# Performance work log

Hardware: AMD Instinct MI355X
Metric: run time of the kernel (lower is better)

The kernel has to match this reference:

```python
import jax, jax.numpy as jnp
import numpy as np

L, B, E = 8192, 2, 1024
H, WS = 16, 256
D = E // H


def setup_inputs() -> dict:
    key = jax.random.key(0)
    ks = jax.random.split(key, 8)
    mk = lambda k: jax.random.normal(k, (E, E), dtype=jnp.float32) * 0.02
    return {
        'query': jax.random.normal(ks[0], (L, B, E), dtype=jnp.float32),
        'key':   jax.random.normal(ks[1], (L, B, E), dtype=jnp.float32),
        'value': jax.random.normal(ks[2], (L, B, E), dtype=jnp.float32),
        'Wq': mk(ks[3]), 'bq': jnp.zeros((E,), jnp.float32),
        'Wk': mk(ks[4]), 'bk': jnp.zeros((E,), jnp.float32),
        'Wv': mk(ks[5]), 'bv': jnp.zeros((E,), jnp.float32),
        'Wo': mk(ks[6]), 'bo': jnp.zeros((E,), jnp.float32),
    }


def reference(query, key, value, Wq, bq, Wk, bk, Wv, bv, Wo, bo):
    # Faithful translation, including the original's (B,L,H,D) layout and the
    # raw-memory view(B,H,L//ws,ws,D) reinterpretation of that layout.
    proj = lambda x, W, b: x @ W.T + b
    # (L,B,E) -> (L,B,H,D) -> transpose(0,1) -> (B,L,H,D)
    q = jnp.swapaxes(proj(query, Wq, bq).reshape(L, B, H, D), 0, 1)
    k = jnp.swapaxes(proj(key,   Wk, bk).reshape(L, B, H, D), 0, 1)
    v = jnp.swapaxes(proj(value, Wv, bv).reshape(L, B, H, D), 0, 1)
    # L > ws, L % ws == 0 -> pad_len = 0; contiguous().view == reshape
    nW = L // WS
    q = q.reshape(B, H, nW, WS, D)
    k = k.reshape(B, H, nW, WS, D)
    v = v.reshape(B, H, nW, WS, D)
    attn = jnp.einsum('bhnqd,bhnkd->bhnqk', q, k) / (D ** 0.5)
    attn = jax.nn.softmax(attn, axis=-1)
    out = jnp.einsum('bhnqk,bhnkd->bhnqd', attn, v)  # (B,H,nW,ws,D)
    out = out.reshape(B, H, L, D)
    # transpose(0,1).contiguous().view(L,B,E): reinterpret (H,B,L,D) memory
    out = jnp.swapaxes(out, 0, 1).reshape(L, B, E)
    return out @ Wo.T + bo
```

## Files before the change

kernel.cpp:

```cpp
#include <hip/hip_runtime.h>


typedef _Float16 half8 __attribute__((ext_vector_type(8)));
typedef _Float16 half4 __attribute__((ext_vector_type(4)));
typedef float    f32x4 __attribute__((ext_vector_type(4)));

#define MFMA16(a, b, c) __builtin_amdgcn_mfma_f32_16x16x32_f16((a), (b), (c), 0, 0, 0)
#define VM(n) asm volatile("s_waitcnt vmcnt(" #n ")" ::: "memory")
#define SCHED0 __builtin_amdgcn_sched_barrier(0)
#define LGKM0 do { asm volatile("s_waitcnt lgkmcnt(0)" ::: "memory"); SCHED0; } while (0)
#define BARW do { __builtin_amdgcn_s_barrier(); SCHED0; } while (0)

__device__ inline void gload16(const _Float16* g, _Float16* l) {
  __builtin_amdgcn_global_load_lds(
      (const __attribute__((address_space(1))) void*)g,
      (__attribute__((address_space(3))) void*)l, 16, 0, 0);
}

__device__ inline half8 cvt8(float4 a, float4 b) {
  half8 h = {(_Float16)a.x, (_Float16)a.y, (_Float16)a.z, (_Float16)a.w,
             (_Float16)b.x, (_Float16)b.y, (_Float16)b.z, (_Float16)b.w};
  return h;
}

__global__ __launch_bounds__(256) void cvtw_k(const float* __restrict__ s0,
                                              const float* __restrict__ s1,
                                              const float* __restrict__ s2,
                                              const float* __restrict__ s3,
                                              _Float16* __restrict__ d) {
  const float* s = blockIdx.y == 0 ? s0 : blockIdx.y == 1 ? s1 : blockIdx.y == 2 ? s2 : s3;
  _Float16* dst = d + (size_t)blockIdx.y * (1 << 20);
  int i = (blockIdx.x * 256 + threadIdx.x) * 8;
  float4 a = *(const float4*)(s + i);
  float4 b = *(const float4*)(s + i + 4);
  *(half8*)(dst + i) = cvt8(a, b);
}

template <int A_F32, int OUT_F32>
__device__ __attribute__((always_inline)) void gemm8p_body(
    const void* __restrict__ A, const _Float16* __restrict__ Bw,
    const float* __restrict__ bias, void* __restrict__ Cout) {
  constexpr int K = 1024, NN = 1024, NT = 16;
  __shared__ alignas(16) _Float16 SH[65536];
  const int tid = threadIdx.x, lane = tid & 63, wave = tid >> 6;
  const int r15 = lane & 15, g = lane >> 4;
  const int wr = wave >> 2, wc = wave & 3;
  const int m0 = blockIdx.x * 256, n0 = blockIdx.y * 256;

  const int sp = tid >> 3;
  const int sv = (tid & 7) ^ (sp & 7);
  const int srow = 2 * sp + (sv >> 2);
  const int scol = (sv & 3) * 8;
  const int sdst = tid * 8;

  const int rp = r15 >> 1, rsub = r15 & 1;
  const int rslot = ((rsub * 4 + g) ^ rp) * 8;

  const float* Af = (const float*)A;
  const _Float16* Ah = (const _Float16*)A;

  f32x4 acc[8][4] = {};
  float4 fr0[4], fr1[4];
  half8 af[4], bf[4];

#define A_REGION(buf, kh) (&SH[(buf)*16384 + (kh)*8192])
#define B_REGION(buf, kh) (&SH[32768 + (buf)*16384 + (kh)*8192])

#define STAGE_B(t, buf, kh)                                                    \
  do {                                                                         \
    const _Float16* _s = Bw + (size_t)(n0 + srow) * K + (t)*64 + (kh)*32 + scol; \
    gload16(_s, B_REGION(buf, kh) + sdst);                                     \
    gload16(_s + (size_t)128 * K, B_REGION(buf, kh) + sdst + 4096);            \
  } while (0)

#define STAGE_A16(t, buf, kh)                                                  \
  do {                                                                         \
    const _Float16* _s = Ah + (size_t)(m0 + srow) * K + (t)*64 + (kh)*32 + scol; \
    gload16(_s, A_REGION(buf, kh) + sdst);                                     \
    gload16(_s + (size_t)128 * K, A_REGION(buf, kh) + sdst + 4096);            \
  } while (0)

#define A_ISSUE(fr, t, kh)                                                     \
  do {                                                                         \
    const float* _s = Af + (size_t)(m0 + srow) * K + (t)*64 + (kh)*32 + scol;  \
    fr[0] = ((const float4*)_s)[0];                                            \
    fr[1] = ((const float4*)_s)[1];                                            \
    const float* _s2 = _s + (size_t)128 * K;                                   \
    fr[2] = ((const float4*)_s2)[0];                                           \
    fr[3] = ((const float4*)_s2)[1];                                           \
  } while (0)

#define A_WRITE(fr, buf, kh)                                                   \
  do {                                                                         \
    *(half8*)&A_REGION(buf, kh)[sdst] = cvt8(fr[0], fr[1]);                    \
    *(half8*)&A_REGION(buf, kh)[sdst + 4096] = cvt8(fr[2], fr[3]);             \
  } while (0)

#define READ_AF(buf, kk, MH)                                                   \
  do {                                                                         \
    _Float16* _b = A_REGION(buf, kk);                                          \
    int _pb = (wr * 64 + (MH)*32 + rp) * 64 + rslot;                           \
    af[0] = *(half8*)&_b[_pb];                                                 \
    af[1] = *(half8*)&_b[_pb + 512];                                           \
    af[2] = *(half8*)&_b[_pb + 1024];                                          \
    af[3] = *(half8*)&_b[_pb + 1536];                                          \
  } while (0)

#define READ_BF(buf, kk)                                                       \
  do {                                                                         \
    _Float16* _b = B_REGION(buf, kk);                                          \
    int _pb = (wc * 32 + rp) * 64 + rslot;                                     \
    bf[0] = *(half8*)&_b[_pb];                                                 \
    bf[1] = *(half8*)&_b[_pb + 512];                                           \
    bf[2] = *(half8*)&_b[_pb + 1024];                                          \
    bf[3] = *(half8*)&_b[_pb + 1536];                                          \
  } while (0)

#define MFMA_Q(MH)                                                             \
  do {                                                                         \
    __builtin_amdgcn_s_setprio(1);                                             \
    _Pragma("unroll") for (int mi = 0; mi < 4; mi++)                           \
        _Pragma("unroll") for (int ni = 0; ni < 4; ni++) acc[(MH)*4 + mi][ni] = \
        MFMA16(af[mi], bf[ni], acc[(MH)*4 + mi][ni]);                          \
    __builtin_amdgcn_s_setprio(0);                                             \
  } while (0)

  if (A_F32) {
    A_ISSUE(fr0, 0, 0);
    A_ISSUE(fr1, 0, 1);
    STAGE_B(0, 0, 0);
    STAGE_B(0, 0, 1);
    VM(8); SCHED0;
    A_WRITE(fr0, 0, 0);
    VM(4); SCHED0;
    A_WRITE(fr1, 0, 1);
    asm volatile("s_waitcnt lgkmcnt(0)" ::: "memory");
  } else {
    STAGE_A16(0, 0, 0);
    STAGE_A16(0, 0, 1);
    STAGE_B(0, 0, 0);
    STAGE_B(0, 0, 1);
  }

  for (int t = 0; t < NT - 1; t++) {
    const int buf = t & 1, nb = buf ^ 1;
    if (A_F32) {
      A_ISSUE(fr0, t + 1, 0);
      VM(6);
    } else {
      STAGE_A16(t + 1, nb, 0);
      VM(4);
    }
    BARW;
    READ_AF(buf, 0, 0);
    READ_BF(buf, 0);
    LGKM0;
    MFMA_Q(0);
    if (A_F32) A_ISSUE(fr1, t + 1, 1);
    else STAGE_A16(t + 1, nb, 1);
    READ_AF(buf, 0, 1);
    LGKM0;
    MFMA_Q(1);
    STAGE_B(t + 1, nb, 0);
    VM(6); SCHED0;
    if (A_F32) A_WRITE(fr0, nb, 0);
    BARW;
    READ_AF(buf, 1, 0);
    READ_BF(buf, 1);
    LGKM0;
    MFMA_Q(0);
    STAGE_B(t + 1, nb, 1);
    if (A_F32) {
      VM(4); SCHED0;
      A_WRITE(fr1, nb, 1);
    }
    READ_AF(buf, 1, 1);
    LGKM0;
    MFMA_Q(1);
  }

  {
    VM(2);
    BARW;
    READ_AF(1, 0, 0);
    READ_BF(1, 0);
    LGKM0;
    MFMA_Q(0);
    READ_AF(1, 0, 1);
    LGKM0;
    MFMA_Q(1);
    VM(0);
    BARW;
    READ_AF(1, 1, 0);
    READ_BF(1, 1);
    LGKM0;
    MFMA_Q(0);
    READ_AF(1, 1, 1);
    LGKM0;
    MFMA_Q(1);
  }

#pragma unroll
  for (int ni = 0; ni < 4; ni++) {
    const int col = n0 + wc * 64 + ni * 16 + r15;
    const float bv = bias[col];
#pragma unroll
    for (int mi8 = 0; mi8 < 8; mi8++) {
      const int rowb = m0 + wr * 128 + mi8 * 16 + g * 4;
#pragma unroll
      for (int r = 0; r < 4; r++) {
        float x = acc[mi8][ni][r] + bv;
        if (OUT_F32)
          ((float*)Cout)[(size_t)(rowb + r) * NN + col] = x;
        else
          ((_Float16*)Cout)[(size_t)(rowb + r) * NN + col] = (_Float16)x;
      }
    }
  }
#undef A_REGION
#undef B_REGION
#undef STAGE_B
#undef STAGE_A16
#undef A_ISSUE
#undef A_WRITE
#undef READ_AF
#undef READ_BF
#undef MFMA_Q
}

__global__ __launch_bounds__(512) void gemm_proj_k(
    const float* __restrict__ Aq, const float* __restrict__ Ak,
    const float* __restrict__ Av, const _Float16* __restrict__ W16,
    const float* __restrict__ bq, const float* __restrict__ bk,
    const float* __restrict__ bv, _Float16* __restrict__ Oq,
    _Float16* __restrict__ Ok, _Float16* __restrict__ Ov) {
  const int z = blockIdx.z;
  const float* A = z == 0 ? Aq : z == 1 ? Ak : Av;
  const float* bias = z == 0 ? bq : z == 1 ? bk : bv;
  _Float16* out = z == 0 ? Oq : z == 1 ? Ok : Ov;
  gemm8p_body<1, 0>((const void*)A, W16 + ((size_t)z << 20), bias, (void*)out);
}

__global__ __launch_bounds__(512) void gemm_out_k(const _Float16* __restrict__ A,
                                                  const _Float16* __restrict__ Bw,
                                                  const float* __restrict__ bias,
                                                  float* __restrict__ Cout) {
  gemm8p_body<0, 1>((const void*)A, Bw, bias, (void*)Cout);
}

__global__ __launch_bounds__(256) void vtrans_k(const _Float16* __restrict__ Vp,
                                                _Float16* __restrict__ Vt) {
  const int c = blockIdx.x, b = blockIdx.y;
  __shared__ alignas(16) _Float16 Vl[256 * 64];
  const int tid = threadIdx.x;
  const int l0 = c * 16;
#pragma unroll
  for (int i = 0; i < 8; i++) {
    int q = tid + i * 256;
    int w = q >> 3, ck = q & 7;
    int ls = l0 + (w >> 4), h = w & 15;
    half8 v = *(const half8*)(Vp + (size_t)(ls * 2 + b) * 1024 + h * 64 + ck * 8);
    *(half8*)&Vl[w * 64 + (ck ^ (w & 7)) * 8] = v;
  }
  __syncthreads();
  const int d = tid >> 2, kcq = tid & 3;
  const size_t obase = ((size_t)(b * 512 + c) * 64 + d) * 256 + kcq * 64;
#pragma unroll
  for (int i8 = 0; i8 < 8; i8++) {
    half8 v;
#pragma unroll
    for (int j = 0; j < 8; j++) {
      int k = kcq * 64 + i8 * 8 + j;
      v[j] = Vl[k * 64 + (((d >> 3) ^ (k & 7)) * 8) + (d & 7)];
    }
    *(half8*)(Vt + obase + i8 * 8) = v;
  }
}

__global__ __launch_bounds__(512) void attn_win_k(const _Float16* __restrict__ Qp,
                                                  const _Float16* __restrict__ Kp,
                                                  const _Float16* __restrict__ Vt,
                                                  _Float16* __restrict__ Y) {
  const int c = blockIdx.x, b = blockIdx.y;
  __shared__ alignas(16) _Float16 Kl[256 * 64];
  __shared__ alignas(16) _Float16 Vl[64 * 256];
  const int tid = threadIdx.x, lane = tid & 63, wave = tid >> 6;
  const int i15 = lane & 15, g = lane >> 4;
  const int l0 = c * 16;

#pragma unroll
  for (int i = 0; i < 4; i++) {
    int q = tid + i * 512;
    int w = q >> 3, ck = q & 7;
    int ls = l0 + (w >> 4), h = w & 15;
    half8 v = *(const half8*)(Kp + (size_t)(ls * 2 + b) * 1024 + h * 64 + ck * 8);
    *(half8*)&Kl[w * 64 + (ck ^ (w & 7)) * 8] = v;
  }
  const size_t vb0 = (size_t)(b * 512 + c) * 64 * 256;
#pragma unroll
  for (int i = 0; i < 4; i++) {
    int q = tid + i * 512;
    int d = q >> 5, ck = q & 31;
    half8 v = *(const half8*)(Vt + vb0 + (size_t)d * 256 + ck * 8);
    *(half8*)&Vl[d * 256 + (ck ^ ((d & 7) << 2)) * 8] = v;
  }
  half8 qf[2][2];
#pragma unroll
  for (int wf = 0; wf < 2; wf++)
#pragma unroll
    for (int dh = 0; dh < 2; dh++) {
      int ls = l0 + wave * 2 + wf;
      qf[wf][dh] =
          *(const half8*)(Qp + (size_t)(ls * 2 + b) * 1024 + i15 * 64 + dh * 32 + g * 8);
    }
  __syncthreads();

  f32x4 acc[16][2] = {};
#pragma unroll
  for (int m = 0; m < 16; m++) {
    int row = m * 16 + i15;
    half8 a0 = *(half8*)&Kl[row * 64 + ((g) ^ (i15 & 7)) * 8];
    half8 a1 = *(half8*)&Kl[row * 64 + ((4 + g) ^ (i15 & 7)) * 8];
    acc[m][0] = MFMA16(a0, qf[0][0], acc[m][0]);
    acc[m][0] = MFMA16(a1, qf[0][1], acc[m][0]);
    acc[m][1] = MFMA16(a0, qf[1][0], acc[m][1]);
    acc[m][1] = MFMA16(a1, qf[1][1], acc[m][1]);
  }

#pragma unroll
  for (int wf = 0; wf < 2; wf++) {
    float mx = -3.0e38f;
#pragma unroll
    for (int m = 0; m < 16; m++)
#pragma unroll
      for (int r = 0; r < 4; r++) mx = fmaxf(mx, acc[m][wf][r]);
    mx = fmaxf(mx, __shfl_xor(mx, 16, 64));
    mx = fmaxf(mx, __shfl_xor(mx, 32, 64));
    float sum = 0.f;
#pragma unroll
    for (int m = 0; m < 16; m++)
#pragma unroll
      for (int r = 0; r < 4; r++) {
        float e = __expf((acc[m][wf][r] - mx) * 0.125f);
        acc[m][wf][r] = e;
        sum += e;
      }
    sum += __shfl_xor(sum, 16, 64);
    sum += __shfl_xor(sum, 32, 64);
    float inv = 1.f / sum;
#pragma unroll
    for (int m = 0; m < 16; m++)
#pragma unroll
      for (int r = 0; r < 4; r++) acc[m][wf][r] *= inv;
  }
  __syncthreads();

  _Float16* Pw = &Kl[wave * 2048];
  f32x4 oacc[2][4] = {};
#pragma unroll
  for (int kq = 0; kq < 4; kq++) {
#pragma unroll
    for (int wf = 0; wf < 2; wf++) {
      int rrow = wf * 16 + i15;
#pragma unroll
      for (int ml = 0; ml < 4; ml++) {
        f32x4 pv = acc[kq * 4 + ml][wf];
        half4 h = {(_Float16)pv[0], (_Float16)pv[1], (_Float16)pv[2], (_Float16)pv[3]};
        int ck = ml * 2 + (g >> 1);
        *(half4*)&Pw[rrow * 64 + ((ck ^ (i15 & 7)) * 8) + (g & 1) * 4] = h;
      }
    }
    asm volatile("s_waitcnt lgkmcnt(0)" ::: "memory");
    __builtin_amdgcn_sched_barrier(0);
#pragma unroll
    for (int kfl = 0; kfl < 2; kfl++) {
      half8 pa0 = *(half8*)&Pw[(i15)*64 + (((kfl * 4 + g) ^ (i15 & 7)) * 8)];
      half8 pa1 = *(half8*)&Pw[(16 + i15) * 64 + (((kfl * 4 + g) ^ (i15 & 7)) * 8)];
#pragma unroll
      for (int df = 0; df < 4; df++) {
        int drow = df * 16 + i15;
        half8 vbf =
            *(half8*)&Vl[drow * 256 + (((kq * 8 + kfl * 4 + g) ^ ((i15 & 7) << 2)) * 8)];
        oacc[0][df] = MFMA16(pa0, vbf, oacc[0][df]);
        oacc[1][df] = MFMA16(pa1, vbf, oacc[1][df]);
      }
    }
  }

  const int h2 = c >> 5, n = c & 31;
  const size_t yb = ((size_t)(h2 * 2 + b) * 8192 + (size_t)n * 256) * 64;
#pragma unroll
  for (int wf = 0; wf < 2; wf++)
#pragma unroll
    for (int df = 0; df < 4; df++)
#pragma unroll
      for (int r = 0; r < 4; r++) {
        int w = wave * 32 + wf * 16 + g * 4 + r;
        Y[yb + (size_t)w * 64 + df * 16 + i15] = (_Float16)oacc[wf][df][r];
      }
}

extern "C" void kernel_launch(void* const* d_in, const int* in_sizes, int n_in,
                              void* d_out, int out_size, void* d_ws, size_t ws_size,
                              hipStream_t stream) {
  const float* query = (const float*)d_in[0];
  const float* key_ = (const float*)d_in[1];
  const float* value = (const float*)d_in[2];
  const float* Wq = (const float*)d_in[3];
  const float* bq = (const float*)d_in[4];
  const float* Wk = (const float*)d_in[5];
  const float* bk = (const float*)d_in[6];
  const float* Wv = (const float*)d_in[7];
  const float* bv = (const float*)d_in[8];
  const float* Wo = (const float*)d_in[9];
  const float* bo = (const float*)d_in[10];

  _Float16* ws = (_Float16*)d_ws;
  _Float16* W16 = ws;
  _Float16* W16o = W16 + 3 * (1 << 20);
  _Float16* Vp = ws + 4 * (1 << 20);
  _Float16* Vt = Vp + (1 << 24);
  _Float16* Ybuf = Vp;

  _Float16* Qp = (_Float16*)d_out;
  _Float16* Kp = Qp + (1 << 24);

  cvtw_k<<<dim3(512, 4), 256, 0, stream>>>(Wq, Wk, Wv, Wo, W16);

  gemm_proj_k<<<dim3(64, 4, 3), 512, 0, stream>>>(query, key_, value, W16, bq, bk, bv,
                                                  Qp, Kp, Vp);

  vtrans_k<<<dim3(512, 2), 256, 0, stream>>>(Vp, Vt);
  attn_win_k<<<dim3(512, 2), 512, 0, stream>>>(Qp, Kp, Vt, Ybuf);

  gemm_out_k<<<dim3(64, 4), 512, 0, stream>>>(Ybuf, W16o, bo, (float*)d_out);

  (void)in_sizes; (void)n_in; (void)out_size; (void)ws_size;
}
```

Baseline: 255.0 us.

## Deepen fp32-A register prefetch to two tiles ahead in projection GEMM

The fp32-input path of the projection GEMM now keeps two sets of register staging buffers (even/odd) and issues global loads for tile t+2 while tile t+1's data is converted and written to LDS. The K loop is fully unrolled into 16 tile steps with specialized tail modes and adjusted vmcnt waits. The aim is to hide global-load latency of the fp32 activations behind more MFMA work. It doubles the staging registers, which could raise register pressure and lower occupancy, and it hardcodes 16 K-tiles.

```diff
diff --git a/kernel.cpp b/kernel.cpp
--- a/kernel.cpp
+++ b/kernel.cpp
@@ -60,7 +60,6 @@
   const _Float16* Ah = (const _Float16*)A;
 
   f32x4 acc[8][4] = {};
-  float4 fr0[4], fr1[4];
   half8 af[4], bf[4];
 
 #define A_REGION(buf, kh) (&SH[(buf)*16384 + (kh)*8192])
@@ -125,79 +124,97 @@
     __builtin_amdgcn_s_setprio(0);                                             \
   } while (0)
 
+#define TILE_F32(T, BUF, FRX0, FRX1, FRY0, FRY1, MODE)                         \
+  {                                                                            \
+    const int _t = (T), _nb = (BUF) ^ 1;                                       \
+                                                                      \
+    if (MODE < 2) STAGE_B(_t + 1, _nb, 0);                                     \
+    if (MODE < 2) { VM(12); } else { VM(2); }                                  \
+    SCHED0; BARW;                                                              \
+    READ_AF(BUF, 0, 0); READ_BF(BUF, 0); LGKM0; MFMA_Q(0);                     \
+                                                                      \
+    if (MODE == 0) A_ISSUE(FRX0, _t + 2, 0);                                   \
+    READ_AF(BUF, 0, 1); LGKM0; MFMA_Q(1);                                      \
+                                                                      \
+    if (MODE < 2) STAGE_B(_t + 1, _nb, 1);                                     \
+    if (MODE < 2) A_WRITE(FRY0, _nb, 0);                                       \
+    if (MODE == 0) { VM(12); } else if (MODE == 1) { VM(8); } else { VM(0); }  \
+    SCHED0; BARW;                                                              \
+    READ_AF(BUF, 1, 0); READ_BF(BUF, 1); LGKM0; MFMA_Q(0);                     \
+                                                                      \
+    if (MODE == 0) A_ISSUE(FRX1, _t + 2, 1);                                   \
+    if (MODE < 2) A_WRITE(FRY1, _nb, 1);                                       \
+    READ_AF(BUF, 1, 1); LGKM0; MFMA_Q(1);                                      \
+  }
+
   if (A_F32) {
-    A_ISSUE(fr0, 0, 0);
-    A_ISSUE(fr1, 0, 1);
+    float4 frE0[4], frE1[4], frO0[4], frO1[4];
+    A_ISSUE(frE0, 0, 0);
+    A_ISSUE(frE1, 0, 1);
     STAGE_B(0, 0, 0);
     STAGE_B(0, 0, 1);
-    VM(8); SCHED0;
-    A_WRITE(fr0, 0, 0);
-    VM(4); SCHED0;
-    A_WRITE(fr1, 0, 1);
-    asm volatile("s_waitcnt lgkmcnt(0)" ::: "memory");
+    A_WRITE(frE0, 0, 0);
+    A_WRITE(frE1, 0, 1);
+    A_ISSUE(frO0, 1, 0);
+    A_ISSUE(frO1, 1, 1);
+    LGKM0;
+    for (int tt = 0; tt < 7; tt++) {
+      const int te = tt * 2;
+      TILE_F32(te, 0, frE0, frE1, frO0, frO1, 0);
+      TILE_F32(te + 1, 1, frO0, frO1, frE0, frE1, 0);
+    }
+    TILE_F32(14, 0, frE0, frE1, frO0, frO1, 1);
+    TILE_F32(15, 1, frO0, frO1, frE0, frE1, 2);
   } else {
     STAGE_A16(0, 0, 0);
     STAGE_A16(0, 0, 1);
     STAGE_B(0, 0, 0);
     STAGE_B(0, 0, 1);
-  }
-
-  for (int t = 0; t < NT - 1; t++) {
-    const int buf = t & 1, nb = buf ^ 1;
-    if (A_F32) {
-      A_ISSUE(fr0, t + 1, 0);
-      VM(6);
-    } else {
+    for (int t = 0; t < NT - 1; t++) {
+      const int buf = t & 1, nb = buf ^ 1;
       STAGE_A16(t + 1, nb, 0);
       VM(4);
-    }
-    BARW;
-    READ_AF(buf, 0, 0);
-    READ_BF(buf, 0);
-    LGKM0;
-    MFMA_Q(0);
-    if (A_F32) A_ISSUE(fr1, t + 1, 1);
-    else STAGE_A16(t + 1, nb, 1);
-    READ_AF(buf, 0, 1);
-    LGKM0;
-    MFMA_Q(1);
-    STAGE_B(t + 1, nb, 0);
-    VM(6); SCHED0;
-    if (A_F32) A_WRITE(fr0, nb, 0);
-    BARW;
-    READ_AF(buf, 1, 0);
-    READ_BF(buf, 1);
-    LGKM0;
-    MFMA_Q(0);
-    STAGE_B(t + 1, nb, 1);
-    if (A_F32) {
-      VM(4); SCHED0;
-      A_WRITE(fr1, nb, 1);
-    }
-    READ_AF(buf, 1, 1);
-    LGKM0;
-    MFMA_Q(1);
-  }
-
-  {
-    VM(2);
-    BARW;
-    READ_AF(1, 0, 0);
-    READ_BF(1, 0);
-    LGKM0;
-    MFMA_Q(0);
-    READ_AF(1, 0, 1);
-    LGKM0;
-    MFMA_Q(1);
-    VM(0);
-    BARW;
-    READ_AF(1, 1, 0);
-    READ_BF(1, 1);
-    LGKM0;
-    MFMA_Q(0);
-    READ_AF(1, 1, 1);
-    LGKM0;
-    MFMA_Q(1);
+      SCHED0; BARW;
+      READ_AF(buf, 0, 0);
+      READ_BF(buf, 0);
+      LGKM0;
+      MFMA_Q(0);
+      STAGE_A16(t + 1, nb, 1);
+      READ_AF(buf, 0, 1);
+      LGKM0;
+      MFMA_Q(1);
+      STAGE_B(t + 1, nb, 0);
+      VM(6);
+      SCHED0; BARW;
+      READ_AF(buf, 1, 0);
+      READ_BF(buf, 1);
+      LGKM0;
+      MFMA_Q(0);
+      STAGE_B(t + 1, nb, 1);
+      READ_AF(buf, 1, 1);
+      LGKM0;
+      MFMA_Q(1);
+    }
+    {
+      VM(2);
+      SCHED0; BARW;
+      READ_AF(1, 0, 0);
+      READ_BF(1, 0);
+      LGKM0;
+      MFMA_Q(0);
+      READ_AF(1, 0, 1);
+      LGKM0;
+      MFMA_Q(1);
+      VM(0);
+      SCHED0; BARW;
+      READ_AF(1, 1, 0);
+      READ_BF(1, 1);
+      LGKM0;
+      MFMA_Q(0);
+      READ_AF(1, 1, 1);
+      LGKM0;
+      MFMA_Q(1);
+    }
   }
 
 #pragma unroll
@@ -226,6 +243,7 @@
 #undef READ_AF
 #undef READ_BF
 #undef MFMA_Q
+#undef TILE_F32
 }
 
 __global__ __launch_bounds__(512) void gemm_proj_k(
```

New measurement: 306.4 us. +20.1%, slower.

## Pre-convert activations to fp16 and run projections as separate fp16 GEMMs

Applied to the files above, without the earlier changes.

The projection GEMM no longer loads fp32 activations and converts them to fp16 inside its main loop. Each of query, key and value is now converted to fp16 by a separate kernel into a shared workspace, and that fp16 buffer is fed to the same async-LDS GEMM path already used for the output projection. This removes the register staging and in-loop conversion from the GEMM pipeline. In exchange it adds an extra full read and write pass over every activation. It also replaces the single fused 3-way launch with six launches that run one after another, so each projection GEMM grid is only 256 blocks.

```diff
diff --git a/kernel.cpp b/kernel.cpp
--- a/kernel.cpp
+++ b/kernel.cpp
@@ -21,6 +21,15 @@
   half8 h = {(_Float16)a.x, (_Float16)a.y, (_Float16)a.z, (_Float16)a.w,
              (_Float16)b.x, (_Float16)b.y, (_Float16)b.z, (_Float16)b.w};
   return h;
+}
+
+__global__ __launch_bounds__(256) void cvt_fp16_k(const float* __restrict__ src,
+                                                  _Float16* __restrict__ dst, int n) {
+  int i = (blockIdx.x * 256 + threadIdx.x) * 8;
+  if (i >= n) return;
+  float4 a = *(const float4*)(src + i);
+  float4 b = *(const float4*)(src + i + 4);
+  *(half8*)(dst + i) = cvt8(a, b);
 }
 
 __global__ __launch_bounds__(256) void cvtw_k(const float* __restrict__ s0,
@@ -36,10 +45,11 @@
   *(half8*)(dst + i) = cvt8(a, b);
 }
 
-template <int A_F32, int OUT_F32>
-__device__ __attribute__((always_inline)) void gemm8p_body(
-    const void* __restrict__ A, const _Float16* __restrict__ Bw,
-    const float* __restrict__ bias, void* __restrict__ Cout) {
+template <int OUT_F32>
+__global__ __launch_bounds__(512) void gemm8p_k(const _Float16* __restrict__ Ah,
+                                                const _Float16* __restrict__ Bw,
+                                                const float* __restrict__ bias,
+                                                void* __restrict__ Cout) {
   constexpr int K = 1024, NN = 1024, NT = 16;
   __shared__ alignas(16) _Float16 SH[65536];
   const int tid = threadIdx.x, lane = tid & 63, wave = tid >> 6;
@@ -56,11 +66,7 @@
   const int rp = r15 >> 1, rsub = r15 & 1;
   const int rslot = ((rsub * 4 + g) ^ rp) * 8;
 
-  const float* Af = (const float*)A;
-  const _Float16* Ah = (const _Float16*)A;
-
   f32x4 acc[8][4] = {};
-  float4 fr0[4], fr1[4];
   half8 af[4], bf[4];
 
 #define A_REGION(buf, kh) (&SH[(buf)*16384 + (kh)*8192])
@@ -78,22 +84,6 @@
     const _Float16* _s = Ah + (size_t)(m0 + srow) * K + (t)*64 + (kh)*32 + scol; \
     gload16(_s, A_REGION(buf, kh) + sdst);                                     \
     gload16(_s + (size_t)128 * K, A_REGION(buf, kh) + sdst + 4096);            \
-  } while (0)
-
-#define A_ISSUE(fr, t, kh)                                                     \
-  do {                                                                         \
-    const float* _s = Af + (size_t)(m0 + srow) * K + (t)*64 + (kh)*32 + scol;  \
-    fr[0] = ((const float4*)_s)[0];                                            \
-    fr[1] = ((const float4*)_s)[1];                                            \
-    const float* _s2 = _s + (size_t)128 * K;                                   \
-    fr[2] = ((const float4*)_s2)[0];                                           \
-    fr[3] = ((const float4*)_s2)[1];                                           \
-  } while (0)
-
-#define A_WRITE(fr, buf, kh)                                                   \
-  do {                                                                         \
-    *(half8*)&A_REGION(buf, kh)[sdst] = cvt8(fr[0], fr[1]);                    \
-    *(half8*)&A_REGION(buf, kh)[sdst + 4096] = cvt8(fr[2], fr[3]);             \
   } while (0)
 
 #define READ_AF(buf, kk, MH)                                                   \
@@ -125,63 +115,39 @@
     __builtin_amdgcn_s_setprio(0);                                             \
   } while (0)
 
-  if (A_F32) {
-    A_ISSUE(fr0, 0, 0);
-    A_ISSUE(fr1, 0, 1);
-    STAGE_B(0, 0, 0);
-    STAGE_B(0, 0, 1);
-    VM(8); SCHED0;
-    A_WRITE(fr0, 0, 0);
-    VM(4); SCHED0;
-    A_WRITE(fr1, 0, 1);
-    asm volatile("s_waitcnt lgkmcnt(0)" ::: "memory");
-  } else {
-    STAGE_A16(0, 0, 0);
-    STAGE_A16(0, 0, 1);
-    STAGE_B(0, 0, 0);
-    STAGE_B(0, 0, 1);
-  }
+  STAGE_A16(0, 0, 0);
+  STAGE_A16(0, 0, 1);
+  STAGE_B(0, 0, 0);
+  STAGE_B(0, 0, 1);
 
   for (int t = 0; t < NT - 1; t++) {
     const int buf = t & 1, nb = buf ^ 1;
-    if (A_F32) {
-      A_ISSUE(fr0, t + 1, 0);
-      VM(6);
-    } else {
-      STAGE_A16(t + 1, nb, 0);
-      VM(4);
-    }
-    BARW;
+    STAGE_A16(t + 1, nb, 0);
+    VM(4);
+    SCHED0; BARW;
     READ_AF(buf, 0, 0);
     READ_BF(buf, 0);
     LGKM0;
     MFMA_Q(0);
-    if (A_F32) A_ISSUE(fr1, t + 1, 1);
-    else STAGE_A16(t + 1, nb, 1);
+    STAGE_A16(t + 1, nb, 1);
     READ_AF(buf, 0, 1);
     LGKM0;
     MFMA_Q(1);
     STAGE_B(t + 1, nb, 0);
-    VM(6); SCHED0;
-    if (A_F32) A_WRITE(fr0, nb, 0);
-    BARW;
+    VM(6);
+    SCHED0; BARW;
     READ_AF(buf, 1, 0);
     READ_BF(buf, 1);
     LGKM0;
     MFMA_Q(0);
     STAGE_B(t + 1, nb, 1);
-    if (A_F32) {
-      VM(4); SCHED0;
-      A_WRITE(fr1, nb, 1);
-    }
     READ_AF(buf, 1, 1);
     LGKM0;
     MFMA_Q(1);
   }
-
   {
     VM(2);
-    BARW;
+    SCHED0; BARW;
     READ_AF(1, 0, 0);
     READ_BF(1, 0);
     LGKM0;
@@ -190,7 +156,7 @@
     LGKM0;
     MFMA_Q(1);
     VM(0);
-    BARW;
+    SCHED0; BARW;
     READ_AF(1, 1, 0);
     READ_BF(1, 1);
     LGKM0;
@@ -221,31 +187,9 @@
 #undef B_REGION
 #undef STAGE_B
 #undef STAGE_A16
-#undef A_ISSUE
-#undef A_WRITE
 #undef READ_AF
 #undef READ_BF
 #undef MFMA_Q
-}
-
-__global__ __launch_bounds__(512) void gemm_proj_k(
-    const float* __restrict__ Aq, const float* __restrict__ Ak,
-    const float* __restrict__ Av, const _Float16* __restrict__ W16,
-    const float* __restrict__ bq, const float* __restrict__ bk,
-    const float* __restrict__ bv, _Float16* __restrict__ Oq,
-    _Float16* __restrict__ Ok, _Float16* __restrict__ Ov) {
-  const int z = blockIdx.z;
-  const float* A = z == 0 ? Aq : z == 1 ? Ak : Av;
-  const float* bias = z == 0 ? bq : z == 1 ? bk : bv;
-  _Float16* out = z == 0 ? Oq : z == 1 ? Ok : Ov;
-  gemm8p_body<1, 0>((const void*)A, W16 + ((size_t)z << 20), bias, (void*)out);
-}
-
-__global__ __launch_bounds__(512) void gemm_out_k(const _Float16* __restrict__ A,
-                                                  const _Float16* __restrict__ Bw,
-                                                  const float* __restrict__ bias,
-                                                  float* __restrict__ Cout) {
-  gemm8p_body<0, 1>((const void*)A, Bw, bias, (void*)Cout);
 }
 
 __global__ __launch_bounds__(256) void vtrans_k(const _Float16* __restrict__ Vp,
@@ -417,9 +361,13 @@
 
   _Float16* ws = (_Float16*)d_ws;
   _Float16* W16 = ws;
+  _Float16* W16q = W16;
+  _Float16* W16k = W16 + (1 << 20);
+  _Float16* W16v = W16 + 2 * (1 << 20);
   _Float16* W16o = W16 + 3 * (1 << 20);
-  _Float16* Vp = ws + 4 * (1 << 20);
-  _Float16* Vt = Vp + (1 << 24);
+  _Float16* X16 = ws + 4 * (1 << 20);
+  _Float16* Vp = X16 + (1 << 24);
+  _Float16* Vt = X16;
   _Float16* Ybuf = Vp;
 
   _Float16* Qp = (_Float16*)d_out;
@@ -427,13 +375,21 @@
 
   cvtw_k<<<dim3(512, 4), 256, 0, stream>>>(Wq, Wk, Wv, Wo, W16);
 
-  gemm_proj_k<<<dim3(64, 4, 3), 512, 0, stream>>>(query, key_, value, W16, bq, bk, bv,
-                                                  Qp, Kp, Vp);
+  dim3 gg(64, 4), gb(512);
+
+  cvt_fp16_k<<<8192, 256, 0, stream>>>(query, X16, 1 << 24);
+  gemm8p_k<0><<<gg, gb, 0, stream>>>(X16, W16q, bq, (void*)Qp);
+
+  cvt_fp16_k<<<8192, 256, 0, stream>>>(key_, X16, 1 << 24);
+  gemm8p_k<0><<<gg, gb, 0, stream>>>(X16, W16k, bk, (void*)Kp);
+
+  cvt_fp16_k<<<8192, 256, 0, stream>>>(value, X16, 1 << 24);
+  gemm8p_k<0><<<gg, gb, 0, stream>>>(X16, W16v, bv, (void*)Vp);
 
   vtrans_k<<<dim3(512, 2), 256, 0, stream>>>(Vp, Vt);
   attn_win_k<<<dim3(512, 2), 512, 0, stream>>>(Qp, Kp, Vt, Ybuf);
 
-  gemm_out_k<<<dim3(64, 4), 512, 0, stream>>>(Ybuf, W16o, bo, (float*)d_out);
+  gemm8p_k<1><<<gg, gb, 0, stream>>>(Ybuf, W16o, bo, d_out);
 
   (void)in_sizes; (void)n_in; (void)out_size; (void)ws_size;
 }
```

Result: slower. 272.1 us (+6.7%).
